# Kernel optimization log

Hardware: AMD Instinct MI355X
Metric: run time of the kernel (lower is better)

Reference implementation:

```python
import jax, jax.numpy as jnp
import numpy as np

B, T, C = 8, 2048, 1024
HEAD_SIZE = 64
HEAD_NUM = 0
NUM_HEADS = 16


def setup_inputs() -> dict:
    key = jax.random.key(0)
    k1, k2, k3, k4 = jax.random.split(key, 4)
    x = jax.random.normal(k1, (B, T, C), dtype=jnp.float32)
    s = C ** -0.5  # Linear init scale
    Wq = jax.random.normal(k2, (C, HEAD_SIZE), dtype=jnp.float32) * s
    Wk = jax.random.normal(k3, (C, HEAD_SIZE), dtype=jnp.float32) * s
    Wv = jax.random.normal(k4, (C, HEAD_SIZE), dtype=jnp.float32) * s
    return {"x": x, "Wq": Wq, "Wk": Wk, "Wv": Wv}


def reference(x, Wq, Wk, Wv):
    # single head of self-attention with ALiBi bias + causal mask (dropout in eval mode = identity)
    q = x @ Wq  # [B,T,H]
    k = x @ Wk  # [B,T,H]
    v = x @ Wv  # [B,T,H]
    scale = jnp.float32(HEAD_SIZE) ** -0.5
    t = jnp.arange(T)
    # base_bias[i,j] = j - i, scaled by per-head ALiBi slope
    slope = 2.0 ** (-8.0 * (HEAD_NUM + 1) / NUM_HEADS)
    m = (t[None, :] - t[:, None]).astype(jnp.float32) * slope  # [T,T]
    # note: bias is added BEFORE the 1/sqrt(d) scaling, as in the original
    scores = (jnp.einsum('bqh,bkh->bqk', q, k) + m) * scale  # [B,T,T]
    causal = t[None, :] <= t[:, None]  # [T,T] lower-triangular
    scores = jnp.where(causal, scores, -jnp.inf)
    attn = jax.nn.softmax(scores, axis=-1)
    out = jnp.einsum('bqk,bkh->bqh', attn, v)  # [B,T,H]
    return out
```

## Files before the change

kernel.cpp:

```cpp
#include <hip/hip_runtime.h>
#include <hip/hip_bf16.h>
#include <math.h>

#define B_ 8
#define T_ 2048
#define C_ 1024
#define H_ 64
#define M_ (B_*T_)

typedef __attribute__((ext_vector_type(8))) short bf16x8;
typedef __attribute__((ext_vector_type(4))) float floatx4;

static __device__ __forceinline__ unsigned short f2bf(float f) {
    union { float f; unsigned u; } v; v.f = f;
    unsigned r = v.u + 0x7fffu + ((v.u >> 16) & 1u);
    return (unsigned short)(r >> 16);
}
static __device__ __forceinline__ unsigned short f2bf_fast(float f) {
    union { float f; unsigned u; } v; v.f = f;
    return (unsigned short)((v.u + 0x8000u) >> 16);
}
static __device__ __forceinline__ unsigned pk2h(float lo, float hi) {
    union { float f; unsigned u; } a, b; a.f = lo; b.f = hi;
    return __builtin_amdgcn_perm(b.u + 0x8000u, a.u + 0x8000u, 0x07060302u);
}
static __device__ __forceinline__ bf16x8 cvt8(float4 f0, float4 f1) {
    union { uint4 u; bf16x8 v; } r;
    r.u.x = pk2h(f0.x, f0.y); r.u.y = pk2h(f0.z, f0.w);
    r.u.z = pk2h(f1.x, f1.y); r.u.w = pk2h(f1.z, f1.w);
    return r.v;
}

#define MFMA(a,b,c) __builtin_amdgcn_mfma_f32_16x16x32_bf16((a),(b),(c),0,0,0)

__global__ __launch_bounds__(256) void wprep_kernel(
    const float* __restrict__ Wq, const float* __restrict__ Wk,
    const float* __restrict__ Wv, unsigned short* __restrict__ wt2)
{
    const int f    = blockIdx.x * 256 + threadIdx.x;
    const int nt   = f >> 11;
    const int kc   = (f >> 6) & 31;
    const int lane = f & 63;
    const int l15  = lane & 15, quad = lane >> 4;
    const int col  = nt * 16 + l15;
    const float* W = (col < 64) ? Wq : ((col < 128) ? Wk : Wv);
    const int   cw = col & 63;
    const float sc = (col < 64) ? 0.125f : 1.0f;
    unsigned short o[8];
    #pragma unroll
    for (int j = 0; j < 8; j++) {
        const int kk = kc * 32 + quad * 8 + j;
        o[j] = f2bf(W[(size_t)kk * 64 + cw] * sc);
    }
    *(uint4*)&wt2[(size_t)f * 8] = *(const uint4*)o;
}

__global__ __launch_bounds__(256) void qkv_kernel(
    const float* __restrict__ x, const unsigned short* __restrict__ wt2,
    unsigned short* __restrict__ qo, unsigned short* __restrict__ ko,
    unsigned short* __restrict__ vo)
{
    __shared__ __align__(16) unsigned short es[16 * 200];

    const int t    = threadIdx.x;
    const int w    = t >> 6;
    const int lane = t & 63;
    const int l15  = lane & 15;
    const int quad = lane >> 4;
    const int r0   = blockIdx.x * 16;

    floatx4 acc0 = (floatx4)(0.0f), acc1 = (floatx4)(0.0f), acc2 = (floatx4)(0.0f);

    const float*          xa = x   + (size_t)(r0 + l15) * C_ + quad * 8;
    const unsigned short* wb = wt2 + (size_t)(w * 3) * 32 * 512 + lane * 8;

    #pragma unroll 2
    for (int kc = 0; kc < 16; kc++) {
        const int k0 = kc * 64;
        const float4 x00 = *(const float4*)(xa + k0);
        const float4 x01 = *(const float4*)(xa + k0 + 4);
        const float4 x10 = *(const float4*)(xa + k0 + 32);
        const float4 x11 = *(const float4*)(xa + k0 + 36);
        const bf16x8 b0l = *(const bf16x8*)(wb + (size_t)(0 * 32 + 2 * kc) * 512);
        const bf16x8 b0h = *(const bf16x8*)(wb + (size_t)(0 * 32 + 2 * kc + 1) * 512);
        const bf16x8 b1l = *(const bf16x8*)(wb + (size_t)(1 * 32 + 2 * kc) * 512);
        const bf16x8 b1h = *(const bf16x8*)(wb + (size_t)(1 * 32 + 2 * kc + 1) * 512);
        const bf16x8 b2l = *(const bf16x8*)(wb + (size_t)(2 * 32 + 2 * kc) * 512);
        const bf16x8 b2h = *(const bf16x8*)(wb + (size_t)(2 * 32 + 2 * kc + 1) * 512);
        const bf16x8 a0  = cvt8(x00, x01);
        const bf16x8 a1  = cvt8(x10, x11);
        acc0 = MFMA(a0, b0l, acc0);  acc0 = MFMA(a1, b0h, acc0);
        acc1 = MFMA(a0, b1l, acc1);  acc1 = MFMA(a1, b1h, acc1);
        acc2 = MFMA(a0, b2l, acc2);  acc2 = MFMA(a1, b2h, acc2);
    }

    {
        const floatx4 av[3] = {acc0, acc1, acc2};
        #pragma unroll
        for (int nt = 0; nt < 3; nt++) {
            const int col = w * 48 + nt * 16 + l15;
            #pragma unroll
            for (int r = 0; r < 4; r++)
                es[(quad * 4 + r) * 200 + col] = f2bf(av[nt][r]);
        }
    }
    __syncthreads();

    {
        const int m   = t >> 7;
        const int row = (t >> 3) & 15;
        const int oct = t & 7;
        unsigned short* outp = m ? ko : qo;
        *(uint4*)&outp[(size_t)(r0 + row) * 64 + oct * 8] =
            *(const uint4*)&es[row * 200 + m * 64 + oct * 8];
    }
    {
        const int h  = t >> 2;
        const int j0 = (t & 3) * 4;
        const int bb = r0 >> 11, tt = r0 & 2047;
        __align__(8) unsigned short tmp[4];
        #pragma unroll
        for (int j = 0; j < 4; j++) tmp[j] = es[(j0 + j) * 200 + 128 + h];
        *(uint2*)&vo[((size_t)bb * 64 + h) * 2048 + tt + j0] = *(uint2*)tmp;
    }
}

__global__ __launch_bounds__(256, 2) void attn_kernel(
    const unsigned short* __restrict__ q,
    const unsigned short* __restrict__ k,
    const unsigned short* __restrict__ vT,
    float* __restrict__ out)
{
    __shared__ __align__(16) unsigned char smem[16384 + 512];
    unsigned short* pT  = (unsigned short*)smem;
    float*          Omg = (float*)smem;
    float*          mlg = (float*)(smem + 16384);

    const int t    = threadIdx.x;
    const int w    = t >> 6;
    const int lane = t & 63;
    const int l15  = lane & 15;
    const int quad = lane >> 4;
    const int b    = blockIdx.x & 7;
    const int qt   = 127 - (blockIdx.x >> 3);
    const int q0   = qt * 16;
    const size_t kb = (size_t)b * T_ * 64;

    const bf16x8 qf0 = *(const bf16x8*)&q[kb + (size_t)(q0 + l15) * 64 + quad * 8];
    const bf16x8 qf1 = *(const bf16x8*)&q[kb + (size_t)(q0 + l15) * 64 + 32 + quad * 8];

    floatx4 O[4];
    #pragma unroll
    for (int i = 0; i < 4; i++) O[i] = (floatx4)(0.0f);
    float mrow[4], lrow[4];
    #pragma unroll
    for (int r = 0; r < 4; r++) { mrow[r] = -INFINITY; lrow[r] = 0.0f; }

    const int nk     = q0 + 16;
    const int nsteps = (nk + 63) >> 6;
    const int ns4    = (nsteps + 3) >> 2;
    const int sBeg   = w * ns4;
    const int sEnd   = min(sBeg + ns4, nsteps);
    const float bs   = 0.088388347648318447f;
    const int   ig0  = q0 + quad * 4;
    unsigned short* pw = pT + w * 16 * 72;

    bf16x8 kf[4][2], vf[4][2];
    #define LOADSTEP(dK, dV, jj0)                                              \
        { _Pragma("unroll")                                                    \
          for (int nt = 0; nt < 4; nt++) {                                     \
              _Pragma("unroll")                                                \
              for (int ks = 0; ks < 2; ks++) {                                 \
                  dK[nt][ks] = *(const bf16x8*)                                \
                      &k[kb + (size_t)((jj0) + nt*16 + l15)*64 + ks*32 + quad*8]; \
                  dV[nt][ks] = *(const bf16x8*)                                \
                      &vT[((size_t)b*64 + nt*16 + l15)*2048 + (jj0) + ks*32 + quad*8]; \
              } } }

    if (sBeg < sEnd) LOADSTEP(kf, vf, sBeg * 64)

    #pragma unroll 2
    for (int s = sBeg; s < sEnd; s++) {
        const int j0 = s * 64;

        floatx4 sc[4];
        #pragma unroll
        for (int nt = 0; nt < 4; nt++) {
            floatx4 z = (floatx4)(0.0f);
            z = MFMA(qf0, kf[nt][0], z);
            z = MFMA(qf1, kf[nt][1], z);
            sc[nt] = z;
        }

        bf16x8 kf2[4][2], vf2[4][2];
        const bool more = (s + 1 < sEnd);
        if (more) LOADSTEP(kf2, vf2, (s + 1) * 64)

        #pragma unroll
        for (int r = 0; r < 4; r++) {
            const int ig = ig0 + r;
            float xv[4];
            float mloc = -INFINITY;
            #pragma unroll
            for (int nt = 0; nt < 4; nt++) {
                const int j = j0 + nt * 16 + l15;
                float v2 = sc[nt][r] + (float)(j - ig) * bs;
                if (j > ig) v2 = -INFINITY;
                xv[nt] = v2;
                mloc = fmaxf(mloc, v2);
            }
            #pragma unroll
            for (int off = 1; off < 16; off <<= 1)
                mloc = fmaxf(mloc, __shfl_xor(mloc, off));
            const float mnew = fmaxf(mrow[r], mloc);
            const float mq   = (mnew == -INFINITY) ? 0.0f : mnew;
            const float alpha = __expf(mrow[r] - mq);
            mrow[r] = mnew;
            float ps = 0.0f;
            #pragma unroll
            for (int nt = 0; nt < 4; nt++) {
                const float p = __expf(xv[nt] - mq);
                ps += p;
                pw[(quad * 4 + r) * 72 + nt * 16 + l15] = f2bf_fast(p);
            }
            lrow[r] = lrow[r] * alpha + ps;
            #pragma unroll
            for (int nt = 0; nt < 4; nt++) O[nt][r] *= alpha;
        }

        const bf16x8 pf0 = *(const bf16x8*)&pw[l15 * 72 + quad * 8];
        const bf16x8 pf1 = *(const bf16x8*)&pw[l15 * 72 + 32 + quad * 8];
        #pragma unroll
        for (int nt = 0; nt < 4; nt++) {
            O[nt] = MFMA(pf0, vf[nt][0], O[nt]);
            O[nt] = MFMA(pf1, vf[nt][1], O[nt]);
        }

        if (more) {
            #pragma unroll
            for (int nt = 0; nt < 4; nt++)
                #pragma unroll
                for (int ks = 0; ks < 2; ks++) {
                    kf[nt][ks] = kf2[nt][ks];
                    vf[nt][ks] = vf2[nt][ks];
                }
        }
    }
    #undef LOADSTEP

    #pragma unroll
    for (int r = 0; r < 4; r++)
        #pragma unroll
        for (int off = 1; off < 16; off <<= 1)
            lrow[r] += __shfl_xor(lrow[r], off);

    __syncthreads();

    #pragma unroll
    for (int nt = 0; nt < 4; nt++)
        #pragma unroll
        for (int r = 0; r < 4; r++)
            Omg[w * 1024 + (quad * 4 + r) * 64 + nt * 16 + l15] = O[nt][r];
    if (l15 == 0) {
        #pragma unroll
        for (int r = 0; r < 4; r++) {
            mlg[w * 32 + (quad * 4 + r)]      = mrow[r];
            mlg[w * 32 + 16 + (quad * 4 + r)] = lrow[r];
        }
    }
    __syncthreads();

    {
        const int row = t >> 4;
        const int hq  = (t & 15) << 2;
        float mstar = -INFINITY;
        #pragma unroll
        for (int w2 = 0; w2 < 4; w2++)
            mstar = fmaxf(mstar, mlg[w2 * 32 + row]);
        floatx4 oa = (floatx4)(0.0f);
        float lsum = 0.0f;
        #pragma unroll
        for (int w2 = 0; w2 < 4; w2++) {
            const float wg = __expf(mlg[w2 * 32 + row] - mstar);
            lsum += wg * mlg[w2 * 32 + 16 + row];
            const floatx4 ov = *(const floatx4*)&Omg[w2 * 1024 + row * 64 + hq];
            oa += wg * ov;
        }
        const float inv = 1.0f / lsum;
        *(floatx4*)&out[kb + (size_t)(q0 + row) * 64 + hq] = oa * inv;
    }
}

extern "C" void kernel_launch(void* const* d_in, const int* in_sizes, int n_in,
                              void* d_out, int out_size, void* d_ws, size_t ws_size,
                              hipStream_t stream) {
    (void)in_sizes; (void)n_in; (void)out_size; (void)ws_size;
    const float* x  = (const float*)d_in[0];
    const float* Wq = (const float*)d_in[1];
    const float* Wk = (const float*)d_in[2];
    const float* Wv = (const float*)d_in[3];
    float* out = (float*)d_out;

    unsigned short* wt2 = (unsigned short*)d_ws;
    unsigned short* qw  = wt2 + 196608;
    unsigned short* kw  = qw + (size_t)M_ * H_;
    unsigned short* vw  = kw + (size_t)M_ * H_;

    wprep_kernel<<<96, 256, 0, stream>>>(Wq, Wk, Wv, wt2);
    qkv_kernel<<<M_ / 16, 256, 0, stream>>>(x, wt2, qw, kw, vw);
    attn_kernel<<<B_ * 128, 256, 0, stream>>>(qw, kw, vw, out);
}
```

Baseline: 169.8 us.

## Enlarge QKV and attention row tiles to reuse weights and K/V

The QKV projection now processes 64 rows per block. x tiles are staged through double-buffered LDS and weight fragments are prefetched, so each weight load serves four M-tiles instead of one. The attention kernel handles 32 query rows per block instead of 16, so each K/V fragment load feeds two query tiles. This halves grid sizes and raises register and LDS use, which may lower occupancy and worsen causal load balance across blocks.

```diff
diff --git a/kernel.cpp b/kernel.cpp
--- a/kernel.cpp
+++ b/kernel.cpp
@@ -60,69 +60,128 @@
     unsigned short* __restrict__ qo, unsigned short* __restrict__ ko,
     unsigned short* __restrict__ vo)
 {
-    __shared__ __align__(16) unsigned short es[16 * 200];
+    __shared__ __align__(16) unsigned short smem[64 * 200];
+    #define XS_(buf) (smem + (buf) * 4608)
 
     const int t    = threadIdx.x;
     const int w    = t >> 6;
     const int lane = t & 63;
     const int l15  = lane & 15;
     const int quad = lane >> 4;
-    const int r0   = blockIdx.x * 16;
-
-    floatx4 acc0 = (floatx4)(0.0f), acc1 = (floatx4)(0.0f), acc2 = (floatx4)(0.0f);
-
-    const float*          xa = x   + (size_t)(r0 + l15) * C_ + quad * 8;
+    const int r0   = blockIdx.x * 64;
+
+    const int srow = t >> 2;
+    const int g0   = t & 3;
+    const float* xrow = x + (size_t)(r0 + srow) * C_;
+
     const unsigned short* wb = wt2 + (size_t)(w * 3) * 32 * 512 + lane * 8;
 
-    #pragma unroll 2
-    for (int kc = 0; kc < 16; kc++) {
-        const int k0 = kc * 64;
-        const float4 x00 = *(const float4*)(xa + k0);
-        const float4 x01 = *(const float4*)(xa + k0 + 4);
-        const float4 x10 = *(const float4*)(xa + k0 + 32);
-        const float4 x11 = *(const float4*)(xa + k0 + 36);
-        const bf16x8 b0l = *(const bf16x8*)(wb + (size_t)(0 * 32 + 2 * kc) * 512);
-        const bf16x8 b0h = *(const bf16x8*)(wb + (size_t)(0 * 32 + 2 * kc + 1) * 512);
-        const bf16x8 b1l = *(const bf16x8*)(wb + (size_t)(1 * 32 + 2 * kc) * 512);
-        const bf16x8 b1h = *(const bf16x8*)(wb + (size_t)(1 * 32 + 2 * kc + 1) * 512);
-        const bf16x8 b2l = *(const bf16x8*)(wb + (size_t)(2 * 32 + 2 * kc) * 512);
-        const bf16x8 b2h = *(const bf16x8*)(wb + (size_t)(2 * 32 + 2 * kc + 1) * 512);
-        const bf16x8 a0  = cvt8(x00, x01);
-        const bf16x8 a1  = cvt8(x10, x11);
-        acc0 = MFMA(a0, b0l, acc0);  acc0 = MFMA(a1, b0h, acc0);
-        acc1 = MFMA(a0, b1l, acc1);  acc1 = MFMA(a1, b1h, acc1);
-        acc2 = MFMA(a0, b2l, acc2);  acc2 = MFMA(a1, b2h, acc2);
-    }
-
+    floatx4 acc[4][3];
+    #pragma unroll
+    for (int mt = 0; mt < 4; mt++)
+        #pragma unroll
+        for (int nt = 0; nt < 3; nt++) acc[mt][nt] = (floatx4)(0.0f);
+
+    bf16x8 wcur[6];
     {
-        const floatx4 av[3] = {acc0, acc1, acc2};
+        #pragma unroll
+        for (int j = 0; j < 2; j++) {
+            const int g = g0 + 4 * j;
+            const float4 f0 = *(const float4*)(xrow + g * 8);
+            const float4 f1 = *(const float4*)(xrow + g * 8 + 4);
+            *(bf16x8*)(XS_(0) + srow * 72 + g * 8) = cvt8(f0, f1);
+        }
+        #pragma unroll
+        for (int nt = 0; nt < 3; nt++)
+            #pragma unroll
+            for (int ks = 0; ks < 2; ks++)
+                wcur[nt * 2 + ks] = *(const bf16x8*)(wb + (size_t)(nt * 32 + ks) * 512);
+    }
+    __syncthreads();
+
+    for (int c = 0; c < 16; c++) {
+        const int buf = c & 1;
+
+        float4 xn[4];
+        bf16x8 wn[6];
+        if (c < 15) {
+            const int k1 = (c + 1) * 64;
+            #pragma unroll
+            for (int j = 0; j < 2; j++) {
+                const int g = g0 + 4 * j;
+                xn[j * 2 + 0] = *(const float4*)(xrow + k1 + g * 8);
+                xn[j * 2 + 1] = *(const float4*)(xrow + k1 + g * 8 + 4);
+            }
+            #pragma unroll
+            for (int nt = 0; nt < 3; nt++)
+                #pragma unroll
+                for (int ks = 0; ks < 2; ks++)
+                    wn[nt * 2 + ks] = *(const bf16x8*)
+                        (wb + (size_t)(nt * 32 + 2 * (c + 1) + ks) * 512);
+        }
+
+        #pragma unroll
+        for (int ks = 0; ks < 2; ks++) {
+            bf16x8 af[4];
+            #pragma unroll
+            for (int mt = 0; mt < 4; mt++)
+                af[mt] = *(const bf16x8*)
+                    (XS_(buf) + (mt * 16 + l15) * 72 + ks * 32 + quad * 8);
+            #pragma unroll
+            for (int mt = 0; mt < 4; mt++)
+                #pragma unroll
+                for (int nt = 0; nt < 3; nt++)
+                    acc[mt][nt] = MFMA(af[mt], wcur[nt * 2 + ks], acc[mt][nt]);
+        }
+
+        if (c < 15) {
+            #pragma unroll
+            for (int j = 0; j < 2; j++) {
+                const int g = g0 + 4 * j;
+                *(bf16x8*)(XS_(buf ^ 1) + srow * 72 + g * 8) =
+                    cvt8(xn[j * 2 + 0], xn[j * 2 + 1]);
+            }
+            #pragma unroll
+            for (int i = 0; i < 6; i++) wcur[i] = wn[i];
+        }
+        __syncthreads();
+    }
+
+    #pragma unroll
+    for (int mt = 0; mt < 4; mt++)
         #pragma unroll
         for (int nt = 0; nt < 3; nt++) {
             const int col = w * 48 + nt * 16 + l15;
             #pragma unroll
             for (int r = 0; r < 4; r++)
-                es[(quad * 4 + r) * 200 + col] = f2bf(av[nt][r]);
-        }
-    }
+                smem[(mt * 16 + quad * 4 + r) * 200 + col] = f2bf(acc[mt][nt][r]);
+        }
     __syncthreads();
 
     {
-        const int m   = t >> 7;
-        const int row = (t >> 3) & 15;
-        const int oct = t & 7;
-        unsigned short* outp = m ? ko : qo;
-        *(uint4*)&outp[(size_t)(r0 + row) * 64 + oct * 8] =
-            *(const uint4*)&es[row * 200 + m * 64 + oct * 8];
+        #pragma unroll
+        for (int i = 0; i < 2; i++) {
+            const int fo  = t + i * 256;
+            const int row = fo >> 3;
+            const int oct = fo & 7;
+            *(uint4*)&qo[(size_t)(r0 + row) * 64 + oct * 8] =
+                *(const uint4*)&smem[row * 200 + oct * 8];
+            *(uint4*)&ko[(size_t)(r0 + row) * 64 + oct * 8] =
+                *(const uint4*)&smem[row * 200 + 64 + oct * 8];
+        }
     }
     {
-        const int h  = t >> 2;
-        const int j0 = (t & 3) * 4;
+        const int h = t >> 2, ts = (t & 3) * 16;
         const int bb = r0 >> 11, tt = r0 & 2047;
-        __align__(8) unsigned short tmp[4];
-        #pragma unroll
-        for (int j = 0; j < 4; j++) tmp[j] = es[(j0 + j) * 200 + 128 + h];
-        *(uint2*)&vo[((size_t)bb * 64 + h) * 2048 + tt + j0] = *(uint2*)tmp;
-    }
+        unsigned short tmp[16];
+        #pragma unroll
+        for (int j = 0; j < 16; j++) tmp[j] = smem[(ts + j) * 200 + 128 + h];
+        #pragma unroll
+        for (int j = 0; j < 2; j++)
+            *(uint4*)&vo[((size_t)bb * 64 + h) * 2048 + tt + ts + j * 8] =
+                *(uint4*)&tmp[j * 8];
+    }
+    #undef XS_
 }
 
 __global__ __launch_bounds__(256, 2) void attn_kernel(
@@ -131,10 +190,10 @@
     const unsigned short* __restrict__ vT,
     float* __restrict__ out)
 {
-    __shared__ __align__(16) unsigned char smem[16384 + 512];
+    __shared__ __align__(16) unsigned char smem[32768 + 1024];
     unsigned short* pT  = (unsigned short*)smem;
     float*          Omg = (float*)smem;
-    float*          mlg = (float*)(smem + 16384);
+    float*          mlg = (float*)(smem + 32768);
 
     const int t    = threadIdx.x;
     const int w    = t >> 6;
@@ -142,28 +201,34 @@
     const int l15  = lane & 15;
     const int quad = lane >> 4;
     const int b    = blockIdx.x & 7;
-    const int qt   = 127 - (blockIdx.x >> 3);
-    const int q0   = qt * 16;
+    const int qt   = 63 - (blockIdx.x >> 3);
+    const int q0   = qt * 32;
     const size_t kb = (size_t)b * T_ * 64;
 
-    const bf16x8 qf0 = *(const bf16x8*)&q[kb + (size_t)(q0 + l15) * 64 + quad * 8];
-    const bf16x8 qf1 = *(const bf16x8*)&q[kb + (size_t)(q0 + l15) * 64 + 32 + quad * 8];
-
-    floatx4 O[4];
-    #pragma unroll
-    for (int i = 0; i < 4; i++) O[i] = (floatx4)(0.0f);
-    float mrow[4], lrow[4];
-    #pragma unroll
-    for (int r = 0; r < 4; r++) { mrow[r] = -INFINITY; lrow[r] = 0.0f; }
-
-    const int nk     = q0 + 16;
-    const int nsteps = (nk + 63) >> 6;
+    bf16x8 qf[2][2];
+    #pragma unroll
+    for (int rt = 0; rt < 2; rt++)
+        #pragma unroll
+        for (int ks = 0; ks < 2; ks++)
+            qf[rt][ks] = *(const bf16x8*)
+                &q[kb + (size_t)(q0 + rt * 16 + l15) * 64 + ks * 32 + quad * 8];
+
+    floatx4 O[2][4];
+    float mrow[2][4], lrow[2][4];
+    #pragma unroll
+    for (int rt = 0; rt < 2; rt++) {
+        #pragma unroll
+        for (int nt = 0; nt < 4; nt++) O[rt][nt] = (floatx4)(0.0f);
+        #pragma unroll
+        for (int r = 0; r < 4; r++) { mrow[rt][r] = -INFINITY; lrow[rt][r] = 0.0f; }
+    }
+
+    const int nsteps = (q0 + 32 + 63) >> 6;
     const int ns4    = (nsteps + 3) >> 2;
     const int sBeg   = w * ns4;
     const int sEnd   = min(sBeg + ns4, nsteps);
     const float bs   = 0.088388347648318447f;
-    const int   ig0  = q0 + quad * 4;
-    unsigned short* pw = pT + w * 16 * 72;
+    unsigned short* pw = pT + w * 32 * 72;
 
     bf16x8 kf[4][2], vf[4][2];
     #define LOADSTEP(dK, dV, jj0)                                              \
@@ -179,61 +244,67 @@
 
     if (sBeg < sEnd) LOADSTEP(kf, vf, sBeg * 64)
 
-    #pragma unroll 2
     for (int s = sBeg; s < sEnd; s++) {
         const int j0 = s * 64;
 
-        floatx4 sc[4];
-        #pragma unroll
-        for (int nt = 0; nt < 4; nt++) {
-            floatx4 z = (floatx4)(0.0f);
-            z = MFMA(qf0, kf[nt][0], z);
-            z = MFMA(qf1, kf[nt][1], z);
-            sc[nt] = z;
-        }
+        floatx4 sc[2][4];
+        #pragma unroll
+        for (int rt = 0; rt < 2; rt++)
+            #pragma unroll
+            for (int nt = 0; nt < 4; nt++) {
+                floatx4 z = (floatx4)(0.0f);
+                z = MFMA(qf[rt][0], kf[nt][0], z);
+                z = MFMA(qf[rt][1], kf[nt][1], z);
+                sc[rt][nt] = z;
+            }
 
         bf16x8 kf2[4][2], vf2[4][2];
         const bool more = (s + 1 < sEnd);
         if (more) LOADSTEP(kf2, vf2, (s + 1) * 64)
 
         #pragma unroll
-        for (int r = 0; r < 4; r++) {
-            const int ig = ig0 + r;
-            float xv[4];
-            float mloc = -INFINITY;
+        for (int rt = 0; rt < 2; rt++)
+            #pragma unroll
+            for (int r = 0; r < 4; r++) {
+                const int ig = q0 + rt * 16 + quad * 4 + r;
+                float xv[4];
+                float mloc = -INFINITY;
+                #pragma unroll
+                for (int nt = 0; nt < 4; nt++) {
+                    const int j = j0 + nt * 16 + l15;
+                    float v2 = sc[rt][nt][r] + (float)(j - ig) * bs;
+                    if (j > ig) v2 = -INFINITY;
+                    xv[nt] = v2;
+                    mloc = fmaxf(mloc, v2);
+                }
+                #pragma unroll
+                for (int off = 1; off < 16; off <<= 1)
+                    mloc = fmaxf(mloc, __shfl_xor(mloc, off));
+                const float mnew = fmaxf(mrow[rt][r], mloc);
+                const float mq   = (mnew == -INFINITY) ? 0.0f : mnew;
+                const float alpha = __expf(mrow[rt][r] - mq);
+                mrow[rt][r] = mnew;
+                float ps = 0.0f;
+                #pragma unroll
+                for (int nt = 0; nt < 4; nt++) {
+                    const float p = __expf(xv[nt] - mq);
+                    ps += p;
+                    pw[(rt * 16 + quad * 4 + r) * 72 + nt * 16 + l15] = f2bf_fast(p);
+                }
+                lrow[rt][r] = lrow[rt][r] * alpha + ps;
+                #pragma unroll
+                for (int nt = 0; nt < 4; nt++) O[rt][nt][r] *= alpha;
+            }
+
+        #pragma unroll
+        for (int rt = 0; rt < 2; rt++) {
+            const bf16x8 pf0 = *(const bf16x8*)&pw[(rt * 16 + l15) * 72 + quad * 8];
+            const bf16x8 pf1 = *(const bf16x8*)&pw[(rt * 16 + l15) * 72 + 32 + quad * 8];
             #pragma unroll
             for (int nt = 0; nt < 4; nt++) {
-                const int j = j0 + nt * 16 + l15;
-                float v2 = sc[nt][r] + (float)(j - ig) * bs;
-                if (j > ig) v2 = -INFINITY;
-                xv[nt] = v2;
-                mloc = fmaxf(mloc, v2);
-            }
-            #pragma unroll
-            for (int off = 1; off < 16; off <<= 1)
-                mloc = fmaxf(mloc, __shfl_xor(mloc, off));
-            const float mnew = fmaxf(mrow[r], mloc);
-            const float mq   = (mnew == -INFINITY) ? 0.0f : mnew;
-            const float alpha = __expf(mrow[r] - mq);
-            mrow[r] = mnew;
-            float ps = 0.0f;
-            #pragma unroll
-            for (int nt = 0; nt < 4; nt++) {
-                const float p = __expf(xv[nt] - mq);
-                ps += p;
-                pw[(quad * 4 + r) * 72 + nt * 16 + l15] = f2bf_fast(p);
-            }
-            lrow[r] = lrow[r] * alpha + ps;
-            #pragma unroll
-            for (int nt = 0; nt < 4; nt++) O[nt][r] *= alpha;
-        }
-
-        const bf16x8 pf0 = *(const bf16x8*)&pw[l15 * 72 + quad * 8];
-        const bf16x8 pf1 = *(const bf16x8*)&pw[l15 * 72 + 32 + quad * 8];
-        #pragma unroll
-        for (int nt = 0; nt < 4; nt++) {
-            O[nt] = MFMA(pf0, vf[nt][0], O[nt]);
-            O[nt] = MFMA(pf1, vf[nt][1], O[nt]);
+                O[rt][nt] = MFMA(pf0, vf[nt][0], O[rt][nt]);
+                O[rt][nt] = MFMA(pf1, vf[nt][1], O[rt][nt]);
+            }
         }
 
         if (more) {
@@ -249,45 +320,53 @@
     #undef LOADSTEP
 
     #pragma unroll
-    for (int r = 0; r < 4; r++)
-        #pragma unroll
-        for (int off = 1; off < 16; off <<= 1)
-            lrow[r] += __shfl_xor(lrow[r], off);
+    for (int rt = 0; rt < 2; rt++)
+        #pragma unroll
+        for (int r = 0; r < 4; r++)
+            #pragma unroll
+            for (int off = 1; off < 16; off <<= 1)
+                lrow[rt][r] += __shfl_xor(lrow[rt][r], off);
 
     __syncthreads();
 
     #pragma unroll
-    for (int nt = 0; nt < 4; nt++)
-        #pragma unroll
-        for (int r = 0; r < 4; r++)
-            Omg[w * 1024 + (quad * 4 + r) * 64 + nt * 16 + l15] = O[nt][r];
+    for (int rt = 0; rt < 2; rt++)
+        #pragma unroll
+        for (int nt = 0; nt < 4; nt++)
+            #pragma unroll
+            for (int r = 0; r < 4; r++)
+                Omg[w * 2048 + (rt * 16 + quad * 4 + r) * 64 + nt * 16 + l15]
+                    = O[rt][nt][r];
     if (l15 == 0) {
         #pragma unroll
-        for (int r = 0; r < 4; r++) {
-            mlg[w * 32 + (quad * 4 + r)]      = mrow[r];
-            mlg[w * 32 + 16 + (quad * 4 + r)] = lrow[r];
-        }
+        for (int rt = 0; rt < 2; rt++)
+            #pragma unroll
+            for (int r = 0; r < 4; r++) {
+                mlg[w * 64 + rt * 16 + quad * 4 + r]      = mrow[rt][r];
+                mlg[w * 64 + 32 + rt * 16 + quad * 4 + r] = lrow[rt][r];
+            }
     }
     __syncthreads();
 
     {
-        const int row = t >> 4;
-        const int hq  = (t & 15) << 2;
+        const int row = t >> 3;
+        const int hq  = (t & 7) << 3;
         float mstar = -INFINITY;
         #pragma unroll
         for (int w2 = 0; w2 < 4; w2++)
-            mstar = fmaxf(mstar, mlg[w2 * 32 + row]);
-        floatx4 oa = (floatx4)(0.0f);
+            mstar = fmaxf(mstar, mlg[w2 * 64 + row]);
+        floatx4 oa0 = (floatx4)(0.0f), oa1 = (floatx4)(0.0f);
         float lsum = 0.0f;
         #pragma unroll
         for (int w2 = 0; w2 < 4; w2++) {
-            const float wg = __expf(mlg[w2 * 32 + row] - mstar);
-            lsum += wg * mlg[w2 * 32 + 16 + row];
-            const floatx4 ov = *(const floatx4*)&Omg[w2 * 1024 + row * 64 + hq];
-            oa += wg * ov;
+            const float wg = __expf(mlg[w2 * 64 + row] - mstar);
+            lsum += wg * mlg[w2 * 64 + 32 + row];
+            oa0 += wg * *(const floatx4*)&Omg[w2 * 2048 + row * 64 + hq];
+            oa1 += wg * *(const floatx4*)&Omg[w2 * 2048 + row * 64 + hq + 4];
         }
         const float inv = 1.0f / lsum;
-        *(floatx4*)&out[kb + (size_t)(q0 + row) * 64 + hq] = oa * inv;
+        *(floatx4*)&out[kb + (size_t)(q0 + row) * 64 + hq]     = oa0 * inv;
+        *(floatx4*)&out[kb + (size_t)(q0 + row) * 64 + hq + 4] = oa1 * inv;
     }
 }
 
@@ -307,6 +386,6 @@
     unsigned short* vw  = kw + (size_t)M_ * H_;
 
     wprep_kernel<<<96, 256, 0, stream>>>(Wq, Wk, Wv, wt2);
-    qkv_kernel<<<M_ / 16, 256, 0, stream>>>(x, wt2, qw, kw, vw);
-    attn_kernel<<<B_ * 128, 256, 0, stream>>>(qw, kw, vw, out);
-}
+    qkv_kernel<<<M_ / 64, 256, 0, stream>>>(x, wt2, qw, kw, vw);
+    attn_kernel<<<B_ * 64, 256, 0, stream>>>(qw, kw, vw, out);
+}
```

New measurement: 144.7 us. -14.7%, faster.
